# Performance work log

Hardware: AMD Instinct MI355X
Metric: run time of the kernel (lower is better)

The kernel has to match this reference:

```python
import jax, jax.numpy as jnp
import numpy as np

H = 1024   # hidden_size == memory_size
NH = 4     # num_attention_heads
HD = H // NH
M = 8192   # total memory items
B, S = 4, 2048
EPS = 1e-5


def _ln(x, g, b):
    mu = jnp.mean(x, -1, keepdims=True)
    var = jnp.mean((x - mu) ** 2, -1, keepdims=True)
    return (x - mu) / jnp.sqrt(var + EPS) * g + b


def setup_inputs() -> dict:
    key = jax.random.key(0)
    ks = jax.random.split(key, 16)
    s = 0.02
    return {
        "query_hidden": jax.random.normal(ks[0], (B, S, H), jnp.float32),
        "mem_keys": jax.random.normal(ks[1], (M, H), jnp.float32),
        "importance": jax.random.uniform(ks[2], (M,), jnp.float32),
        "recency": jax.random.uniform(ks[3], (M,), jnp.float32),
        "access_count": jax.random.uniform(ks[4], (M,), jnp.float32),
        "Wq": s * jax.random.normal(ks[5], (H, H), jnp.float32),
        "bq": jnp.zeros((H,), jnp.float32),
        "in_w": s * jax.random.normal(ks[6], (3 * H, H), jnp.float32),
        "in_b": jnp.zeros((3 * H,), jnp.float32),
        "out_w": s * jax.random.normal(ks[7], (H, H), jnp.float32),
        "out_b": jnp.zeros((H,), jnp.float32),
        "gate_w": s * jax.random.normal(ks[8], (H, 2 * H), jnp.float32),
        "gate_b": jnp.zeros((H,), jnp.float32),
        "int_w1": s * jax.random.normal(ks[9], (2 * H, 2 * H), jnp.float32),
        "int_b1": jnp.zeros((2 * H,), jnp.float32),
        "int_ln_g": jnp.ones((2 * H,), jnp.float32),
        "int_ln_b": jnp.zeros((2 * H,), jnp.float32),
        "int_w2": s * jax.random.normal(ks[10], (H, 2 * H), jnp.float32),
        "int_b2": jnp.zeros((H,), jnp.float32),
        "ln1_g": jnp.ones((H,), jnp.float32),
        "ln1_b": jnp.zeros((H,), jnp.float32),
        "ln2_g": jnp.ones((H,), jnp.float32),
        "ln2_b": jnp.zeros((H,), jnp.float32),
        "sel_params": jnp.ones((3,), jnp.float32) / 3.0,
        "top_k": 2048,
    }


def reference(query_hidden, mem_keys, importance, recency, access_count,
              Wq, bq, in_w, in_b, out_w, out_b, gate_w, gate_b,
              int_w1, int_b1, int_ln_g, int_ln_b, int_w2, int_b2,
              ln1_g, ln1_b, ln2_g, ln2_b, sel_params, top_k):
    b, s, _ = query_hidden.shape
    # HTPS selection: softmax-weighted mix of importance / recency / frequency
    w = jax.nn.softmax(sel_params)
    freq = access_count / jnp.max(access_count)
    sel = w[0] * importance + w[1] * recency + w[2] * freq
    _, idx = jax.lax.top_k(sel, top_k)
    mem = mem_keys[idx]                      # [K, H]
    mem_n = _ln(mem, ln1_g, ln1_b)           # layer_norm1 on memory

    q = query_hidden @ Wq.T + bq             # query_proj  [B,S,H]
    wq, wk, wv = in_w[:H], in_w[H:2 * H], in_w[2 * H:]
    bqi, bki, bvi = in_b[:H], in_b[H:2 * H], in_b[2 * H:]
    # Batched MHA: the per-position loop is equivalent to all S queries at once
    Q = (q @ wq.T + bqi).reshape(b, s, NH, HD)
    K = (mem_n @ wk.T + bki).reshape(top_k, NH, HD)   # shared across batch
    V = (mem_n @ wv.T + bvi).reshape(top_k, NH, HD)
    scores = jnp.einsum('bshd,khd->bhsk', Q, K) / jnp.sqrt(jnp.float32(HD))
    attn = jax.nn.softmax(scores, axis=-1)
    ctx = jnp.einsum('bhsk,khd->bshd', attn, V).reshape(b, s, H)
    attn_out = ctx @ out_w.T + out_b

    cat = jnp.concatenate([query_hidden, attn_out], axis=-1)   # [B,S,2H]
    gate = jax.nn.sigmoid(cat @ gate_w.T + gate_b)
    h1 = _ln(cat @ int_w1.T + int_b1, int_ln_g, int_ln_b)
    integ = jax.nn.gelu(h1, approximate=False) @ int_w2.T + int_b2
    return _ln(query_hidden + gate * integ, ln2_g, ln2_b)
```

## Files before the change

kernel.cpp:

```cpp
#include <hip/hip_runtime.h>

#define HDIM 1024
#define MMEM 8192
#define TOPK 2048
#define NROWS 8192
#define LNEPS 1e-5f

typedef unsigned short ushort_t;
typedef __bf16 bf16x8 __attribute__((ext_vector_type(8)));
typedef float f32x4 __attribute__((ext_vector_type(4)));
typedef __attribute__((address_space(1))) const void GVoid;
typedef __attribute__((address_space(3))) void LVoid;

__device__ __forceinline__ ushort_t f2bf(float f) {
    union { float f; unsigned u; } c; c.f = f;
    unsigned r = c.u + 0x7fffu + ((c.u >> 16) & 1u);
    return (ushort_t)(r >> 16);
}
__device__ __forceinline__ float bf2f(ushort_t u) {
    union { unsigned u; float f; } c; c.u = ((unsigned)u) << 16; return c.f;
}
__device__ __forceinline__ float blk_red(float v, int op, float* red) {
    #pragma unroll
    for (int o = 32; o; o >>= 1) {
        float u = __shfl_down(v, o);
        v = op ? fmaxf(v, u) : v + u;
    }
    if ((threadIdx.x & 63) == 0) red[threadIdx.x >> 6] = v;
    __syncthreads();
    float r = op ? fmaxf(fmaxf(red[0], red[1]), fmaxf(red[2], red[3]))
                 : (red[0] + red[1]) + (red[2] + red[3]);
    __syncthreads();
    return r;
}

__global__ __launch_bounds__(256) void topk_rank(const float* __restrict__ sp,
        const float* __restrict__ imp, const float* __restrict__ rec,
        const float* __restrict__ ac, int* __restrict__ idx) {
    __shared__ float s[MMEM];
    __shared__ int pc[256];
    __shared__ float red[4];
    float p0 = sp[0], p1 = sp[1], p2 = sp[2];
    float mx3 = fmaxf(p0, fmaxf(p1, p2));
    float e0 = __expf(p0 - mx3), e1 = __expf(p1 - mx3), e2 = __expf(p2 - mx3);
    float inv3 = 1.f / (e0 + e1 + e2);
    float w0 = e0 * inv3, w1 = e1 * inv3, w2 = e2 * inv3;
    float m = -1e30f;
    for (int i = threadIdx.x; i < MMEM; i += 256) m = fmaxf(m, ac[i]);
    m = blk_red(m, 1, red);
    float rinv = 1.f / m;
    for (int i = threadIdx.x; i < MMEM; i += 256)
        s[i] = w0 * imp[i] + w1 * rec[i] + w2 * (ac[i] * rinv);
    __syncthreads();
    const int li = threadIdx.x & 31;
    const int jc = threadIdx.x >> 5;
    const int i  = blockIdx.x * 32 + li;
    const float si = s[i];
    int cnt = 0;
    const float4* sv = reinterpret_cast<const float4*>(s) + jc * 256;
    #pragma unroll 4
    for (int t = 0; t < 256; ++t) {
        float4 v = sv[t];
        int j0 = jc * 1024 + t * 4;
        cnt += (v.x > si) || (v.x == si && (j0 + 0) < i);
        cnt += (v.y > si) || (v.y == si && (j0 + 1) < i);
        cnt += (v.z > si) || (v.z == si && (j0 + 2) < i);
        cnt += (v.w > si) || (v.w == si && (j0 + 3) < i);
    }
    pc[threadIdx.x] = cnt;
    __syncthreads();
    if (threadIdx.x < 32) {
        int r = 0;
        #pragma unroll
        for (int c = 0; c < 8; ++c) r += pc[c * 32 + threadIdx.x];
        if (r < TOPK) idx[r] = blockIdx.x * 32 + threadIdx.x;
    }
}

__global__ __launch_bounds__(256) void gather_ln(const float* __restrict__ mem_keys,
        const int* __restrict__ idx, const float* __restrict__ g,
        const float* __restrict__ b, ushort_t* __restrict__ out) {
    __shared__ float red[4];
    int src = idx[blockIdx.x] & (MMEM - 1);
    const float* x = mem_keys + (size_t)src * HDIM;
    float4 v = reinterpret_cast<const float4*>(x)[threadIdx.x];
    float s = v.x + v.y + v.z + v.w;
    float ss = v.x*v.x + v.y*v.y + v.z*v.z + v.w*v.w;
    s  = blk_red(s, 0, red);
    ss = blk_red(ss, 0, red);
    float mu = s * (1.f / HDIM);
    float var = ss * (1.f / HDIM) - mu * mu;
    float rstd = rsqrtf(var + LNEPS);
    int c = threadIdx.x * 4;
    ushort4 o;
    o.x = f2bf((v.x - mu) * rstd * g[c+0] + b[c+0]);
    o.y = f2bf((v.y - mu) * rstd * g[c+1] + b[c+1]);
    o.z = f2bf((v.z - mu) * rstd * g[c+2] + b[c+2]);
    o.w = f2bf((v.w - mu) * rstd * g[c+3] + b[c+3]);
    *reinterpret_cast<ushort4*>(out + (size_t)blockIdx.x * HDIM + c) = o;
}

__global__ __launch_bounds__(256) void cvt_all(const float* __restrict__ in_w,
        const float* __restrict__ gate_w, const float* __restrict__ int_w1,
        const float* __restrict__ int_w2, const float* __restrict__ x,
        ushort_t* __restrict__ inw_bf, ushort_t* __restrict__ gw3,
        ushort_t* __restrict__ intw2_bf, ushort_t* __restrict__ xbf) {
    const int b = blockIdx.x;
    const float* src; ushort_t* dst; int rel;
    if      (b < 3072)  { src = in_w;   dst = inw_bf;        rel = b; }
    else if (b < 5120)  { src = gate_w; dst = gw3;           rel = b - 3072; }
    else if (b < 9216)  { src = int_w1; dst = gw3 + 2097152; rel = b - 5120; }
    else if (b < 11264) { src = int_w2; dst = intw2_bf;      rel = b - 9216; }
    else                { src = x;      dst = xbf;           rel = b - 11264; }
    size_t i = ((size_t)rel * 256 + threadIdx.x) * 4;
    float4 v = *reinterpret_cast<const float4*>(src + i);
    ushort4 o = { f2bf(v.x), f2bf(v.y), f2bf(v.z), f2bf(v.w) };
    *reinterpret_cast<ushort4*>(dst + i) = o;
}

__global__ __launch_bounds__(256) void cvt_t2(const float* __restrict__ a,
        const float* __restrict__ b, ushort_t* __restrict__ oa,
        ushort_t* __restrict__ ob) {
    __shared__ ushort_t t[64][65];
    const float* in = blockIdx.z ? b : a;
    ushort_t* out   = blockIdx.z ? ob : oa;
    const int bx = blockIdx.x * 64, by = blockIdx.y * 64;
    const int r = threadIdx.x >> 4, c4 = (threadIdx.x & 15) << 2;
    #pragma unroll
    for (int rr = 0; rr < 64; rr += 16) {
        float4 v = *reinterpret_cast<const float4*>(in + (size_t)(by + r + rr) * 1024 + bx + c4);
        t[r + rr][c4 + 0] = f2bf(v.x);
        t[r + rr][c4 + 1] = f2bf(v.y);
        t[r + rr][c4 + 2] = f2bf(v.z);
        t[r + rr][c4 + 3] = f2bf(v.w);
    }
    __syncthreads();
    #pragma unroll
    for (int rr = 0; rr < 64; rr += 16) {
        const int i = r + rr;
        ushort4 o = { t[c4 + 0][i], t[c4 + 1][i], t[c4 + 2][i], t[c4 + 3][i] };
        *reinterpret_cast<ushort4*>(out + (size_t)(bx + i) * 1024 + by + c4) = o;
    }
}

__global__ __launch_bounds__(256) void bias_folds(const float* __restrict__ in_w,
        const float* __restrict__ bq, const float* __restrict__ in_b,
        const float* __restrict__ gate_w, const float* __restrict__ int_w1,
        const float* __restrict__ gate_b, const float* __restrict__ int_b1,
        const float* __restrict__ out_b, float* __restrict__ beff,
        float* __restrict__ beff3) {
    __shared__ float red[4];
    const int b = blockIdx.x;
    const float* wrow; const float* vec;
    if (b < 1024) { wrow = in_w + (size_t)b * 1024; vec = bq; }
    else {
        const int j = b - 1024;
        wrow = (j < 1024 ? gate_w + (size_t)j * 2048
                         : int_w1 + (size_t)(j - 1024) * 2048) + 1024;
        vec = out_b;
    }
    const float4 wv = reinterpret_cast<const float4*>(wrow)[threadIdx.x];
    const float4 bv = reinterpret_cast<const float4*>(vec)[threadIdx.x];
    float s = wv.x*bv.x + wv.y*bv.y + wv.z*bv.z + wv.w*bv.w;
    s = blk_red(s, 0, red);
    if (threadIdx.x == 0) {
        if (b < 1024) beff[b] = s + in_b[b];
        else {
            const int j = b - 1024;
            beff3[j] = s + (j < 1024 ? gate_b[j] : int_b1[j - 1024]);
        }
    }
}

__global__ __launch_bounds__(256) void ln_gelu(ushort_t* h1,
        const float* __restrict__ g, const float* __restrict__ b) {
    __shared__ float red[4];
    ushort_t* p = h1 + (size_t)blockIdx.x * 2048 + threadIdx.x * 8;
    ushort4 a = reinterpret_cast<const ushort4*>(p)[0];
    ushort4 c = reinterpret_cast<const ushort4*>(p)[1];
    float v[8] = { bf2f(a.x), bf2f(a.y), bf2f(a.z), bf2f(a.w),
                   bf2f(c.x), bf2f(c.y), bf2f(c.z), bf2f(c.w) };
    float s = 0.f, ss = 0.f;
    #pragma unroll
    for (int j = 0; j < 8; ++j) { s += v[j]; ss += v[j]*v[j]; }
    s  = blk_red(s, 0, red);
    ss = blk_red(ss, 0, red);
    float mu = s * (1.f / 2048.f);
    float var = ss * (1.f / 2048.f) - mu * mu;
    float rstd = rsqrtf(var + LNEPS);
    int c0 = threadIdx.x * 8;
    ushort_t o[8];
    #pragma unroll
    for (int j = 0; j < 8; ++j) {
        float xn = (v[j] - mu) * rstd * g[c0 + j] + b[c0 + j];
        float ge = 0.5f * xn * (1.f + erff(xn * 0.70710678118654752f));
        o[j] = f2bf(ge);
    }
    ushort4 o1 = { o[0], o[1], o[2], o[3] };
    ushort4 o2 = { o[4], o[5], o[6], o[7] };
    reinterpret_cast<ushort4*>(p)[0] = o1;
    reinterpret_cast<ushort4*>(p)[1] = o2;
}

__global__ __launch_bounds__(256) void final_ln(const float* __restrict__ x,
        const ushort_t* __restrict__ gate, const ushort_t* __restrict__ integ,
        const float* __restrict__ g, const float* __restrict__ b,
        float* __restrict__ out) {
    __shared__ float red[4];
    size_t base = (size_t)blockIdx.x * HDIM + threadIdx.x * 4;
    float4 xv = *reinterpret_cast<const float4*>(x + base);
    ushort4 gv = *reinterpret_cast<const ushort4*>(gate + base);
    ushort4 iv = *reinterpret_cast<const ushort4*>(integ + base);
    float v[4] = { xv.x + bf2f(gv.x)*bf2f(iv.x), xv.y + bf2f(gv.y)*bf2f(iv.y),
                   xv.z + bf2f(gv.z)*bf2f(iv.z), xv.w + bf2f(gv.w)*bf2f(iv.w) };
    float s = v[0]+v[1]+v[2]+v[3];
    float ss = v[0]*v[0]+v[1]*v[1]+v[2]*v[2]+v[3]*v[3];
    s  = blk_red(s, 0, red);
    ss = blk_red(ss, 0, red);
    float mu = s * (1.f / HDIM);
    float var = ss * (1.f / HDIM) - mu * mu;
    float rstd = rsqrtf(var + LNEPS);
    int c = threadIdx.x * 4;
    float4 o;
    o.x = (v[0] - mu) * rstd * g[c+0] + b[c+0];
    o.y = (v[1] - mu) * rstd * g[c+1] + b[c+1];
    o.z = (v[2] - mu) * rstd * g[c+2] + b[c+2];
    o.w = (v[3] - mu) * rstd * g[c+3] + b[c+3];
    *reinterpret_cast<float4*>(out + base) = o;
}

__global__ __launch_bounds__(256, 2)
void fattn(const ushort_t* __restrict__ Q, const ushort_t* __restrict__ Kb,
           const ushort_t* __restrict__ Vt, ushort_t* __restrict__ ctx)
{
    __shared__ __align__(16) ushort_t Pb[8192];
    __shared__ __align__(16) ushort_t Stg[16384];
    __shared__ float rsum[64];

    const int z1 = blockIdx.y >> 2, z2 = blockIdx.y & 3;
    const int m0 = blockIdx.x * 64;
    const ushort_t* Qp = Q  + (size_t)z1 * 2097152 + z2 * 256;
    const ushort_t* Kp = Kb + z2 * 256;
    const ushort_t* Vp = Vt + (size_t)z2 * 524288;

    const int tid = threadIdx.x;
    const int w = tid >> 6, l = tid & 63;
    const int srow = l >> 3;
    const int scol = ((l & 7) ^ srow) << 3;
    const int l15 = l & 15, lh = l >> 4;

    if (tid < 64) rsum[tid] = 0.f;

    f32x4 oacc[4][4] = {};

    for (int ch = 0; ch < 16; ++ch) {
        f32x4 sacc[4][2] = {};
        for (int k0 = 0; k0 < 256; k0 += 64) {
            #pragma unroll
            for (int i = 0; i < 2; ++i) {
                const int c = i * 4 + w;
                const ushort_t* g = Qp + (size_t)(m0 + c * 8 + srow) * 1024 + k0 + scol;
                __builtin_amdgcn_global_load_lds((GVoid*)g, (LVoid*)(Stg + c * 512), 16, 0, 0);
            }
            #pragma unroll
            for (int i = 0; i < 4; ++i) {
                const int c = i * 4 + w;
                const ushort_t* g = Kp + (size_t)(ch * 128 + c * 8 + srow) * 1024 + k0 + scol;
                __builtin_amdgcn_global_load_lds((GVoid*)g, (LVoid*)(Stg + 4096 + c * 512), 16, 0, 0);
            }
            __syncthreads();
            #pragma unroll
            for (int kk = 0; kk < 2; ++kk) {
                bf16x8 af[4], bv[2];
                #pragma unroll
                for (int m = 0; m < 4; ++m) {
                    const int row = m * 16 + l15;
                    const int cb = ((kk * 64) + lh * 16) ^ ((row & 7) << 4);
                    af[m] = *reinterpret_cast<const bf16x8*>(
                        reinterpret_cast<const char*>(Stg) + row * 128 + cb);
                }
                #pragma unroll
                for (int n = 0; n < 2; ++n) {
                    const int row = w * 32 + n * 16 + l15;
                    const int cb = ((kk * 64) + lh * 16) ^ ((row & 7) << 4);
                    bv[n] = *reinterpret_cast<const bf16x8*>(
                        reinterpret_cast<const char*>(Stg) + 8192 + row * 128 + cb);
                }
                __builtin_amdgcn_s_setprio(1);
                #pragma unroll
                for (int m = 0; m < 4; ++m)
                    #pragma unroll
                    for (int n = 0; n < 2; ++n)
                        sacc[m][n] = __builtin_amdgcn_mfma_f32_16x16x32_bf16(
                            af[m], bv[n], sacc[m][n], 0, 0, 0);
                __builtin_amdgcn_s_setprio(0);
            }
            __syncthreads();
        }
        #pragma unroll
        for (int m = 0; m < 4; ++m) {
            float ps[4] = {0.f, 0.f, 0.f, 0.f};
            #pragma unroll
            for (int n = 0; n < 2; ++n) {
                const int pcol = w * 32 + n * 16 + l15;
                #pragma unroll
                for (int j = 0; j < 4; ++j) {
                    const int prow = m * 16 + lh * 4 + j;
                    float e = __expf(sacc[m][n][j] * 0.0625f);
                    ps[j] += e;
                    const int cb = (pcol * 2) ^ ((prow & 7) << 4);
                    *reinterpret_cast<ushort_t*>(
                        reinterpret_cast<char*>(Pb) + prow * 256 + cb) = f2bf(e);
                }
            }
            #pragma unroll
            for (int j = 0; j < 4; ++j) {
                float s = ps[j];
                s += __shfl_xor(s, 1); s += __shfl_xor(s, 2);
                s += __shfl_xor(s, 4); s += __shfl_xor(s, 8);
                if (l15 == 0) atomicAdd(&rsum[m * 16 + lh * 4 + j], s);
            }
        }
        #pragma unroll
        for (int ks = 0; ks < 128; ks += 64) {
            #pragma unroll
            for (int i = 0; i < 8; ++i) {
                const int c = i * 4 + w;
                const ushort_t* g = Vp + (size_t)(c * 8 + srow) * 2048 + ch * 128 + ks + scol;
                __builtin_amdgcn_global_load_lds((GVoid*)g, (LVoid*)(Stg + c * 512), 16, 0, 0);
            }
            __syncthreads();
            #pragma unroll
            for (int kk = 0; kk < 2; ++kk) {
                bf16x8 pa[4], vb[4];
                #pragma unroll
                for (int m = 0; m < 4; ++m) {
                    const int row = m * 16 + l15;
                    const int cb = (ks * 2 + kk * 64 + lh * 16) ^ ((row & 7) << 4);
                    pa[m] = *reinterpret_cast<const bf16x8*>(
                        reinterpret_cast<const char*>(Pb) + row * 256 + cb);
                }
                #pragma unroll
                for (int n = 0; n < 4; ++n) {
                    const int row = w * 64 + n * 16 + l15;
                    const int cb = ((kk * 64) + lh * 16) ^ ((row & 7) << 4);
                    vb[n] = *reinterpret_cast<const bf16x8*>(
                        reinterpret_cast<const char*>(Stg) + row * 128 + cb);
                }
                __builtin_amdgcn_s_setprio(1);
                #pragma unroll
                for (int m = 0; m < 4; ++m)
                    #pragma unroll
                    for (int n = 0; n < 4; ++n)
                        oacc[m][n] = __builtin_amdgcn_mfma_f32_16x16x32_bf16(
                            pa[m], vb[n], oacc[m][n], 0, 0, 0);
                __builtin_amdgcn_s_setprio(0);
            }
            __syncthreads();
        }
    }

    #pragma unroll
    for (int m = 0; m < 4; ++m) {
        float riv[4];
        #pragma unroll
        for (int j = 0; j < 4; ++j)
            riv[j] = 1.f / rsum[m * 16 + lh * 4 + j];
        #pragma unroll
        for (int n = 0; n < 4; ++n) {
            const int dcol = w * 64 + n * 16 + l15;
            #pragma unroll
            for (int j = 0; j < 4; ++j) {
                const int row = m * 16 + lh * 4 + j;
                const size_t off = (size_t)(z1 * 2048 + m0 + row) * 1024 + z2 * 256 + dcol;
                ctx[off] = f2bf(oacc[m][n][j] * riv[j]);
            }
        }
    }
}

template<int EPI, int BIAS, int SPLIT>
__global__ __launch_bounds__(256, 2)
void gemm_bt(const ushort_t* __restrict__ A, const ushort_t* __restrict__ B,
             const ushort_t* __restrict__ A2, const ushort_t* __restrict__ B2,
             int lda2, int ldb2,
             const float* __restrict__ bias, void* __restrict__ Cv,
             void* __restrict__ Cv2, const float* __restrict__ bias2,
             int K, int lda, int ldb, int ldc,
             long long sA1, long long sA2s, long long sAz,
             long long sB1, long long sB2s, long long sBz,
             long long sC1, long long sC2s, long long sCz,
             int z2n, int zbase, float scale)
{
    __shared__ __align__(16) ushort_t As[8192];
    __shared__ __align__(16) ushort_t Bs[8192];
    const int zz = blockIdx.z;
    const int zg = zz + zbase;
    const int z1 = zg / z2n, z2 = zg - z1 * z2n;
    A += (size_t)(z1 * sA1 + z2 * sA2s + zz * sAz);
    B += (size_t)(z1 * sB1 + z2 * sB2s + zz * sBz);
    const size_t cOff = (size_t)(z1 * sC1 + z2 * sC2s + zz * sCz);

    const int nwg = gridDim.x * gridDim.y;
    const int wg  = blockIdx.y * gridDim.x + blockIdx.x;
    const int q8  = nwg >> 3, r8 = nwg & 7;
    const int xcd = wg & 7, lo = wg >> 3;
    const int wgid = (xcd < r8 ? xcd * (q8 + 1) : r8 * (q8 + 1) + (xcd - r8) * q8) + lo;
    const int m0 = (wgid / gridDim.x) * 128, n0 = (wgid % gridDim.x) * 128;

    const int tid = threadIdx.x;
    const int w = tid >> 6, l = tid & 63;
    const int wm = w >> 1, wn = w & 1;

    f32x4 acc[4][4] = {};
    const int srow = l >> 3;
    const int scol = ((l & 7) ^ srow) << 3;

    for (int k0 = 0; k0 < K; k0 += 64) {
        const ushort_t* Ab = A; const ushort_t* Bb = B;
        int la = lda, lb = ldb, kk0 = k0;
        if (SPLIT && k0 >= 1024) { Ab = A2; Bb = B2; la = lda2; lb = ldb2; kk0 = k0 - 1024; }
        #pragma unroll
        for (int i = 0; i < 4; ++i) {
            const int c = i * 4 + w;
            const int row = c * 8 + srow;
            const ushort_t* ga = Ab + (size_t)(m0 + row) * la + (kk0 + scol);
            const ushort_t* gb = Bb + (size_t)(n0 + row) * lb + (kk0 + scol);
            __builtin_amdgcn_global_load_lds((GVoid*)ga, (LVoid*)(As + c * 512), 16, 0, 0);
            __builtin_amdgcn_global_load_lds((GVoid*)gb, (LVoid*)(Bs + c * 512), 16, 0, 0);
        }
        __syncthreads();
        #pragma unroll
        for (int kk = 0; kk < 2; ++kk) {
            bf16x8 af[4], bfv[4];
            #pragma unroll
            for (int m = 0; m < 4; ++m) {
                const int row = wm * 64 + m * 16 + (l & 15);
                const int cb = ((kk * 64) + ((l >> 4) * 16)) ^ ((row & 7) << 4);
                af[m] = *reinterpret_cast<const bf16x8*>(
                    reinterpret_cast<const char*>(As) + row * 128 + cb);
            }
            #pragma unroll
            for (int n = 0; n < 4; ++n) {
                const int row = wn * 64 + n * 16 + (l & 15);
                const int cb = ((kk * 64) + ((l >> 4) * 16)) ^ ((row & 7) << 4);
                bfv[n] = *reinterpret_cast<const bf16x8*>(
                    reinterpret_cast<const char*>(Bs) + row * 128 + cb);
            }
            #pragma unroll
            for (int m = 0; m < 4; ++m)
                #pragma unroll
                for (int n = 0; n < 4; ++n)
                    acc[m][n] = __builtin_amdgcn_mfma_f32_16x16x32_bf16(
                        af[m], bfv[n], acc[m][n], 0, 0, 0);
        }
        __syncthreads();
    }

    #pragma unroll
    for (int m = 0; m < 4; ++m) {
        const int grow = m0 + wm * 64 + m * 16 + ((l >> 4) << 2);
        #pragma unroll
        for (int n = 0; n < 4; ++n) {
            const int gcol = n0 + wn * 64 + n * 16 + (l & 15);
            float bc = (BIAS == 1) ? bias[gcol] : 0.f;
            #pragma unroll
            for (int j = 0; j < 4; ++j) {
                if (EPI == 3) {
                    float v = acc[m][n][j];
                    if (gcol < 1024) {
                        v += bias[gcol];
                        v = 1.f / (1.f + __expf(-v));
                        ((ushort_t*)Cv)[(size_t)(grow + j) * ldc + gcol] = f2bf(v);
                    } else {
                        v += bias2[gcol - 1024];
                        ((ushort_t*)Cv2)[(size_t)(grow + j) * 2048 + (gcol - 1024)] = f2bf(v);
                    }
                } else {
                    float v = acc[m][n][j] * scale;
                    if (BIAS == 1) v += bc;
                    if (BIAS == 2) v += bias[grow + j];
                    if (EPI == 2) v = 1.f / (1.f + __expf(-v));
                    const size_t off = cOff + (size_t)(grow + j) * ldc + gcol;
                    if (EPI == 1) ((ushort_t*)Cv)[off] = f2bf(v);
                    else          ((float*)Cv)[off]    = v;
                }
            }
        }
    }
}

extern "C" void kernel_launch(void* const* d_in, const int* in_sizes, int n_in,
                              void* d_out, int out_size, void* d_ws, size_t ws_size,
                              hipStream_t stream) {
    const float* x          = (const float*)d_in[0];
    const float* mem_keys   = (const float*)d_in[1];
    const float* importance = (const float*)d_in[2];
    const float* recency    = (const float*)d_in[3];
    const float* access_cnt = (const float*)d_in[4];
    const float* Wq         = (const float*)d_in[5];
    const float* bq         = (const float*)d_in[6];
    const float* in_w       = (const float*)d_in[7];
    const float* in_b       = (const float*)d_in[8];
    const float* out_w      = (const float*)d_in[9];
    const float* out_b      = (const float*)d_in[10];
    const float* gate_w     = (const float*)d_in[11];
    const float* gate_b     = (const float*)d_in[12];
    const float* int_w1     = (const float*)d_in[13];
    const float* int_b1     = (const float*)d_in[14];
    const float* int_ln_g   = (const float*)d_in[15];
    const float* int_ln_b   = (const float*)d_in[16];
    const float* int_w2     = (const float*)d_in[17];
    const float* int_b2     = (const float*)d_in[18];
    const float* ln1_g      = (const float*)d_in[19];
    const float* ln1_b      = (const float*)d_in[20];
    const float* ln2_g      = (const float*)d_in[21];
    const float* ln2_b      = (const float*)d_in[22];
    const float* sel_params = (const float*)d_in[23];

    char* ws = (char*)d_ws;
    size_t off = 0;
    auto alloc = [&](size_t bytes) -> char* {
        char* p = ws + off;
        off = (off + bytes + 255) & ~(size_t)255;
        return p;
    };

    int*      idx      = (int*)alloc(TOPK * 4);
    float*    beff     = (float*)alloc(1024 * 4);
    float*    beff3    = (float*)alloc(3072 * 4);
    ushort_t* wqT_bf   = (ushort_t*)alloc((size_t)1048576 * 2);
    ushort_t* outwT_bf = (ushort_t*)alloc((size_t)1048576 * 2);
    ushort_t* weff_bf  = (ushort_t*)alloc((size_t)1048576 * 2);
    ushort_t* inw_bf   = (ushort_t*)alloc((size_t)3145728 * 2);
    ushort_t* gw3      = (ushort_t*)alloc((size_t)6291456 * 2);
    ushort_t* wfold3   = (ushort_t*)alloc((size_t)3145728 * 2);
    ushort_t* intw2_bf = (ushort_t*)alloc((size_t)2097152 * 2);
    ushort_t* mem_n    = (ushort_t*)alloc((size_t)TOPK * HDIM * 2);
    ushort_t* Kbuf     = (ushort_t*)alloc((size_t)TOPK * HDIM * 2);
    ushort_t* Vt       = (ushort_t*)alloc((size_t)HDIM * TOPK * 2);
    ushort_t* xbf      = (ushort_t*)alloc((size_t)NROWS * HDIM * 2);
    ushort_t* Qbuf     = (ushort_t*)alloc((size_t)NROWS * HDIM * 2);
    ushort_t* h1       = (ushort_t*)alloc((size_t)NROWS * 2048 * 2);
    ushort_t* ctx      = (ushort_t*)alloc((size_t)NROWS * HDIM * 2);
    ushort_t* integ    = ctx;
    ushort_t* gatev    = (ushort_t*)alloc((size_t)NROWS * HDIM * 2);

    cvt_t2<<<dim3(16,16,2), 256, 0, stream>>>(Wq, out_w, wqT_bf, outwT_bf);
    cvt_all<<<19456, 256, 0, stream>>>(in_w, gate_w, int_w1, int_w2, x,
                                       inw_bf, gw3, intw2_bf, xbf);
    bias_folds<<<4096, 256, 0, stream>>>(in_w, bq, in_b, gate_w, int_w1,
                                         gate_b, int_b1, out_b, beff, beff3);

    gemm_bt<1,0,0><<<dim3(8,8,1), 256, 0, stream>>>(inw_bf, wqT_bf,
        nullptr, nullptr, 0, 0, nullptr, weff_bf, nullptr, nullptr,
        1024, 1024, 1024, 1024, 0,0,0, 0,0,0, 0,0,0, 1, 0, 1.f);
    gemm_bt<1,0,0><<<dim3(8,24,1), 256, 0, stream>>>(gw3 + 1024, outwT_bf,
        nullptr, nullptr, 0, 0, nullptr, wfold3, nullptr, nullptr,
        1024, 2048, 1024, 1024, 0,0,0, 0,0,0, 0,0,0, 1, 0, 1.f);

    topk_rank<<<MMEM/32, 256, 0, stream>>>(sel_params, importance, recency,
                                           access_cnt, idx);
    gather_ln<<<TOPK, 256, 0, stream>>>(mem_keys, idx, ln1_g, ln1_b, mem_n);

    gemm_bt<1,1,0><<<dim3(8,64,1), 256, 0, stream>>>(xbf, weff_bf,
        nullptr, nullptr, 0, 0, beff, Qbuf, nullptr, nullptr,
        1024, 1024, 1024, 1024, 0,0,0, 0,0,0, 0,0,0, 1, 0, 1.f);
    gemm_bt<1,1,0><<<dim3(8,16,1), 256, 0, stream>>>(mem_n, inw_bf + 1048576,
        nullptr, nullptr, 0, 0, in_b + 1024, Kbuf, nullptr, nullptr,
        1024, 1024, 1024, 1024, 0,0,0, 0,0,0, 0,0,0, 1, 0, 1.f);
    gemm_bt<1,2,0><<<dim3(16,8,1), 256, 0, stream>>>(inw_bf + 2097152, mem_n,
        nullptr, nullptr, 0, 0, in_b + 2048, Vt, nullptr, nullptr,
        1024, 1024, 1024, 2048, 0,0,0, 0,0,0, 0,0,0, 1, 0, 1.f);

    fattn<<<dim3(32,16), 256, 0, stream>>>(Qbuf, Kbuf, Vt, ctx);

    gemm_bt<3,0,1><<<dim3(24,64,1), 256, 0, stream>>>(xbf, gw3,
        ctx, wfold3, 1024, 1024, beff3, gatev, h1, beff3 + 1024,
        2048, 1024, 2048, 1024, 0,0,0, 0,0,0, 0,0,0, 1, 0, 1.f);

    ln_gelu<<<NROWS, 256, 0, stream>>>(h1, int_ln_g, int_ln_b);
    gemm_bt<1,1,0><<<dim3(8,64,1), 256, 0, stream>>>(h1, intw2_bf,
        nullptr, nullptr, 0, 0, int_b2, integ, nullptr, nullptr,
        2048, 2048, 2048, 1024, 0,0,0, 0,0,0, 0,0,0, 1, 0, 1.f);
    final_ln<<<NROWS, 256, 0, stream>>>(x, gatev, integ, ln2_g, ln2_b, (float*)d_out);
}
```

Before: 537.2 us.

## Split attention over key halves and add a combine kernel

The attention kernel is split along the key dimension into two halves using a third grid axis. Each half writes unnormalized partial outputs in bf16, along with per-row softmax sums, into scratch memory that reuses the h1 buffer. A new combine kernel adds the two partials and divides by the total sum. Launch bounds are raised to request three blocks per CU, aiming for more in-flight blocks. The cost is an extra pass that reads and writes the full context tensor, an extra rounding to bf16 before normalization, and possible register pressure from the tighter launch bound.

Result: slower. 650.8 us (+21.2%).

```diff
diff --git a/kernel.cpp b/kernel.cpp
--- a/kernel.cpp
+++ b/kernel.cpp
@@ -229,15 +229,17 @@
     *reinterpret_cast<float4*>(out + base) = o;
 }
 
-__global__ __launch_bounds__(256, 2)
+__global__ __launch_bounds__(256, 3)
 void fattn(const ushort_t* __restrict__ Q, const ushort_t* __restrict__ Kb,
-           const ushort_t* __restrict__ Vt, ushort_t* __restrict__ ctx)
+           const ushort_t* __restrict__ Vt, ushort_t* __restrict__ opart,
+           float* __restrict__ rsumg)
 {
     __shared__ __align__(16) ushort_t Pb[8192];
     __shared__ __align__(16) ushort_t Stg[16384];
     __shared__ float rsum[64];
 
     const int z1 = blockIdx.y >> 2, z2 = blockIdx.y & 3;
+    const int zh = blockIdx.z;
     const int m0 = blockIdx.x * 64;
     const ushort_t* Qp = Q  + (size_t)z1 * 2097152 + z2 * 256;
     const ushort_t* Kp = Kb + z2 * 256;
@@ -253,7 +255,7 @@
 
     f32x4 oacc[4][4] = {};
 
-    for (int ch = 0; ch < 16; ++ch) {
+    for (int ch = zh * 8; ch < zh * 8 + 8; ++ch) {
         f32x4 sacc[4][2] = {};
         for (int k0 = 0; k0 < 256; k0 += 64) {
             #pragma unroll
@@ -360,12 +362,9 @@
         }
     }
 
+    ushort_t* op = opart + (size_t)zh * 8388608;
     #pragma unroll
     for (int m = 0; m < 4; ++m) {
-        float riv[4];
-        #pragma unroll
-        for (int j = 0; j < 4; ++j)
-            riv[j] = 1.f / rsum[m * 16 + lh * 4 + j];
         #pragma unroll
         for (int n = 0; n < 4; ++n) {
             const int dcol = w * 64 + n * 16 + l15;
@@ -373,10 +372,30 @@
             for (int j = 0; j < 4; ++j) {
                 const int row = m * 16 + lh * 4 + j;
                 const size_t off = (size_t)(z1 * 2048 + m0 + row) * 1024 + z2 * 256 + dcol;
-                ctx[off] = f2bf(oacc[m][n][j] * riv[j]);
-            }
-        }
-    }
+                op[off] = f2bf(oacc[m][n][j]);
+            }
+        }
+    }
+    if (tid < 64)
+        rsumg[(size_t)zh * 32768 + blockIdx.y * 2048 + m0 + tid] = rsum[tid];
+}
+
+__global__ __launch_bounds__(256) void attn_combine(const ushort_t* __restrict__ op,
+        const float* __restrict__ rsumg, ushort_t* __restrict__ ctx) {
+    const int R = blockIdx.x;
+    const int c = threadIdx.x * 4;
+    const int z1 = R >> 11, z2 = c >> 8;
+    const int zi = (z1 * 4 + z2) * 2048 + (R & 2047);
+    const float r = 1.f / (rsumg[zi] + rsumg[32768 + zi]);
+    const size_t o = (size_t)R * 1024 + c;
+    ushort4 a = *reinterpret_cast<const ushort4*>(op + o);
+    ushort4 b = *reinterpret_cast<const ushort4*>(op + 8388608 + o);
+    ushort4 ov;
+    ov.x = f2bf((bf2f(a.x) + bf2f(b.x)) * r);
+    ov.y = f2bf((bf2f(a.y) + bf2f(b.y)) * r);
+    ov.z = f2bf((bf2f(a.z) + bf2f(b.z)) * r);
+    ov.w = f2bf((bf2f(a.w) + bf2f(b.w)) * r);
+    *reinterpret_cast<ushort4*>(ctx + o) = ov;
 }
 
 template<int EPI, int BIAS, int SPLIT>
@@ -529,6 +548,7 @@
     int*      idx      = (int*)alloc(TOPK * 4);
     float*    beff     = (float*)alloc(1024 * 4);
     float*    beff3    = (float*)alloc(3072 * 4);
+    float*    rsumg    = (float*)alloc((size_t)2 * 32768 * 4);
     ushort_t* wqT_bf   = (ushort_t*)alloc((size_t)1048576 * 2);
     ushort_t* outwT_bf = (ushort_t*)alloc((size_t)1048576 * 2);
     ushort_t* weff_bf  = (ushort_t*)alloc((size_t)1048576 * 2);
@@ -542,6 +562,7 @@
     ushort_t* xbf      = (ushort_t*)alloc((size_t)NROWS * HDIM * 2);
     ushort_t* Qbuf     = (ushort_t*)alloc((size_t)NROWS * HDIM * 2);
     ushort_t* h1       = (ushort_t*)alloc((size_t)NROWS * 2048 * 2);
+    ushort_t* opart    = h1;
     ushort_t* ctx      = (ushort_t*)alloc((size_t)NROWS * HDIM * 2);
     ushort_t* integ    = ctx;
     ushort_t* gatev    = (ushort_t*)alloc((size_t)NROWS * HDIM * 2);
@@ -573,7 +594,8 @@
         nullptr, nullptr, 0, 0, in_b + 2048, Vt, nullptr, nullptr,
         1024, 1024, 1024, 2048, 0,0,0, 0,0,0, 0,0,0, 1, 0, 1.f);
 
-    fattn<<<dim3(32,16), 256, 0, stream>>>(Qbuf, Kbuf, Vt, ctx);
+    fattn<<<dim3(32,16,2), 256, 0, stream>>>(Qbuf, Kbuf, Vt, opart, rsumg);
+    attn_combine<<<NROWS, 256, 0, stream>>>(opart, rsumg, ctx);
 
     gemm_bt<3,0,1><<<dim3(24,64,1), 256, 0, stream>>>(xbf, gw3,
         ctx, wfold3, 1024, 1024, beff3, gatev, h1, beff3 + 1024,
```
